# Kernel optimization log

Measured on AMD Instinct MI355X. Metric: run time of the kernel, lower is better.

## Reference

```python
import jax, jax.numpy as jnp
import numpy as np

B, HW, D, CL, K, V, NL, H = 16, 4096, 512, 768, 512, 512, 32, 8
EPS = 1e-5

def conv1d(x, w, b):
    # 1x1 Conv1d: x (B, Cin, L), w (Cout, Cin), b (Cout,)
    return jnp.einsum('oi,bil->bol', w, x) + b[:, None]

def inorm(x):
    # InstanceNorm1d (affine=False, biased var) over the length dim per channel
    m = jnp.mean(x, axis=-1, keepdims=True)
    v = jnp.var(x, axis=-1, keepdims=True)
    return (x - m) / jnp.sqrt(v + EPS)

def _forward(x, l, l_mask, w_vis, b_vis, w_langp, b_langp, w_q, b_q, w_k, b_k,
             w_v, b_v, w_lv, b_lv, w_W, b_W, w_langW, b_langW,
             w_mm, b_mm, w_langmm, b_langmm):
    xt = x.transpose(0, 2, 1)                       # (B, D, HW)
    mask = l_mask.transpose(0, 2, 1)                # (B, 1, NL)
    vis = jax.nn.gelu(conv1d(xt, w_vis, b_vis), approximate=False)      # (B, D, HW)
    lang = jax.nn.gelu(conv1d(l, w_langp, b_langp), approximate=False)  # (B, CL, NL)

    q = inorm(conv1d(xt, w_q, b_q)).transpose(0, 2, 1)   # (B, HW, K)
    k = conv1d(l, w_k, b_k) * mask                       # (B, K, NL)
    v = conv1d(l, w_v, b_v) * mask                       # (B, V, NL)
    lv = inorm(conv1d(xt, w_lv, b_lv))                   # (B, CL, HW)

    q = q.reshape(B, HW, H, K // H).transpose(0, 2, 1, 3)   # (B, H, HW, dk)
    k = k.reshape(B, H, K // H, NL)
    v = v.reshape(B, H, V // H, NL)
    lv = lv.reshape(B, H, CL // H, HW)

    # note: scale uses FULL key_channels (as in the torch code), mask bias added once
    sim = jnp.einsum('bhqd,bhdn->bhqn', q, k) * (K ** -0.5)
    sim = sim + (10000.0 * mask[:, :, None, :] - 10000.0)    # (B, H, HW, NL)

    att = jax.nn.softmax(sim, axis=-1)                         # image -> lang
    latt = jax.nn.softmax(sim.transpose(0, 1, 3, 2), axis=-1)  # lang -> image

    lang_out = jnp.einsum('bhnq,bhcq->bhcn', latt, lv).reshape(B, CL, NL) * mask
    lang_out = inorm(conv1d(lang_out, w_langW, b_langW))       # (B, CL, NL)

    out = jnp.einsum('bhqn,bhdn->bqhd', att, v).reshape(B, HW, V)
    vis_out = inorm(conv1d(out.transpose(0, 2, 1), w_W, b_W))  # (B, V, HW)

    mm = jax.nn.gelu(conv1d(vis * vis_out, w_mm, b_mm), approximate=False)
    lang_mm = jax.nn.gelu(conv1d(lang * lang_out, w_langmm, b_langmm), approximate=False)
    return mm.transpose(0, 2, 1), lang_mm.transpose(0, 2, 1)   # (B,HW,V), (B,NL,CL)

def setup_inputs():
    key = jax.random.key(0)
    ks = jax.random.split(key, 24)
    inp = {}
    inp['x'] = jax.random.normal(ks[0], (B, HW, D), jnp.float32)
    inp['l'] = jax.random.normal(ks[1], (B, CL, NL), jnp.float32)
    lengths = jax.random.randint(ks[2], (B, 1), 5, NL + 1)
    inp['l_mask'] = (jnp.arange(NL)[None, :] < lengths).astype(jnp.float32)[:, :, None]
    specs = [('vis', D, D), ('langp', CL, CL), ('q', K, D), ('k', K, CL),
             ('v', V, CL), ('lv', CL, D), ('W', V, V), ('langW', CL, CL),
             ('mm', V, V), ('langmm', CL, CL)]
    for i, (n, o, ci) in enumerate(specs):
        inp['w_' + n] = jax.random.normal(ks[3 + 2 * i], (o, ci), jnp.float32) / float(np.sqrt(ci))
        inp['b_' + n] = jax.random.normal(ks[4 + 2 * i], (o,), jnp.float32) * 0.01
    return inp

def reference(x, l, l_mask, w_vis, b_vis, w_langp, b_langp, w_q, b_q, w_k, b_k,
              w_v, b_v, w_lv, b_lv, w_W, b_W, w_langW, b_langW,
              w_mm, b_mm, w_langmm, b_langmm):
    return _forward(x, l, l_mask, w_vis, b_vis, w_langp, b_langp, w_q, b_q, w_k, b_k,
                    w_v, b_v, w_lv, b_lv, w_W, b_W, w_langW, b_langW,
                    w_mm, b_mm, w_langmm, b_langmm)
```

## Files before the change

kernel.cpp:

```cpp
#include <hip/hip_runtime.h>
#include <cstdint>
#include <cstddef>


typedef __bf16 bf16x8 __attribute__((ext_vector_type(8)));
typedef float f32x4 __attribute__((ext_vector_type(4)));
typedef unsigned short ushort8 __attribute__((ext_vector_type(8)));
typedef unsigned short us4 __attribute__((ext_vector_type(4)));

__device__ __forceinline__ float bf2f(unsigned short u) {
  union { unsigned int i; float f; } c; c.i = ((unsigned int)u) << 16; return c.f;
}
__device__ __forceinline__ unsigned short f2bf(float f) {
  union { float f; unsigned int i; } c; c.f = f;
  unsigned int r = c.i + 0x7FFFu + ((c.i >> 16) & 1u);
  return (unsigned short)(r >> 16);
}
__device__ __forceinline__ float gelu_f(float x) {
  return 0.5f * x * (1.f + erff(x * 0.70710678118654752f));
}
__device__ __forceinline__ void gload16(const void* g, void* l) {
  __builtin_amdgcn_global_load_lds(
      (__attribute__((address_space(1))) unsigned int*)g,
      (__attribute__((address_space(3))) unsigned int*)l, 16, 0, 0);
}

constexpr size_t OFF_SRQ  = 0;
constexpr size_t OFF_SRLV = OFF_SRQ  + (size_t)16*512*2*4;
constexpr size_t OFF_SRW  = OFF_SRLV + (size_t)16*768*2*4;
constexpr size_t OFF_LACC = OFF_SRW  + (size_t)16*512*2*4;
constexpr size_t SZ_ZERO  = OFF_LACC + (size_t)16*768*32*4;
constexpr size_t OFF_STQ  = SZ_ZERO;
constexpr size_t OFF_STLV = OFF_STQ  + (size_t)16*512*2*4;
constexpr size_t OFF_STW  = OFF_STLV + (size_t)16*768*2*4;
constexpr size_t OFF_KBUF = OFF_STW  + (size_t)16*512*2*4;
constexpr size_t OFF_VBUF = OFF_KBUF + (size_t)16*512*32*4;
constexpr size_t OFF_LANG = OFF_VBUF + (size_t)16*512*32*4;
constexpr size_t OFF_LMX  = OFF_LANG + (size_t)16*768*32*4;
constexpr size_t OFF_LSM  = OFF_LMX  + (size_t)128*32*4;
constexpr size_t OFF_LNORM= OFF_LSM  + (size_t)128*32*4;
constexpr size_t OFF_P2   = OFF_LNORM+ (size_t)16*768*32*4;
constexpr size_t OFF_PMX  = OFF_P2   + (size_t)16*768*32*4;
constexpr size_t OFF_PSM  = OFF_PMX  + (size_t)32*128*32*4;
constexpr size_t OFF_WB   = OFF_PSM  + (size_t)32*128*32*4;
constexpr size_t OFF_Q    = OFF_WB   + (size_t)1441792*2;
constexpr size_t OFF_LV   = OFF_Q    + (size_t)65536*512*2;
constexpr size_t OFF_SIMB = OFF_LV   + (size_t)65536*768*2;

__global__ __launch_bounds__(256) void cvt_bf16(const float* __restrict__ src,
                                                unsigned short* __restrict__ dst, int n8)
{
  int i = blockIdx.x * 256 + threadIdx.x;
  if (i >= n8) return;
  const f32x4* s = (const f32x4*)(src + (size_t)i * 8);
  f32x4 a = s[0], b = s[1];
  ushort8 o;
#pragma unroll
  for (int j = 0; j < 4; ++j) { o[j] = f2bf(a[j]); o[j + 4] = f2bf(b[j]); }
  *(ushort8*)(dst + (size_t)i * 8) = o;
}

template<bool GELU, bool STATS, bool OUTF32>
__global__ __launch_bounds__(256) void gemm_bt(
    const unsigned short* __restrict__ A, const unsigned short* __restrict__ Wb,
    const float* __restrict__ bias, void* __restrict__ Yout,
    float* __restrict__ statsraw, int N, int Kd)
{
  __shared__ __align__(16) unsigned short As[128 * 64];
  __shared__ __align__(16) unsigned short Bs[128 * 64];
  const int t = threadIdx.x;
  const int wave = t >> 6, lane = t & 63;
  const int ln = lane & 15, quad = lane >> 4;
  const int m0 = blockIdx.x * 128, n0 = blockIdx.y * 128;
  const int wm = (wave >> 1) * 64, wn = (wave & 1) * 64;
  const f32x4 fzero = {0.f, 0.f, 0.f, 0.f};
  f32x4 acc[4][4];
#pragma unroll
  for (int i = 0; i < 4; ++i)
#pragma unroll
    for (int j = 0; j < 4; ++j) acc[i][j] = fzero;
  const int lrow = lane >> 3;
  const int lch  = lane & 7;

  for (int k0 = 0; k0 < Kd; k0 += 64) {
#pragma unroll
    for (int it = 0; it < 4; ++it) {
      int g = wave * 4 + it;
      int row = g * 8 + lrow;
      gload16(A  + (size_t)(m0 + row) * Kd + k0 + lch * 8, &As[g * 512]);
      gload16(Wb + (size_t)(n0 + row) * Kd + k0 + lch * 8, &Bs[g * 512]);
    }
    __syncthreads();
#pragma unroll
    for (int kk = 0; kk < 64; kk += 32) {
      int c = (kk >> 3) + quad;
      bf16x8 af[4], bfr[4];
#pragma unroll
      for (int i = 0; i < 4; ++i)
        af[i] = *(const bf16x8*)&As[(wm + i * 16 + ln) * 64 + c * 8];
#pragma unroll
      for (int j = 0; j < 4; ++j)
        bfr[j] = *(const bf16x8*)&Bs[(wn + j * 16 + ln) * 64 + c * 8];
#pragma unroll
      for (int i = 0; i < 4; ++i)
#pragma unroll
        for (int j = 0; j < 4; ++j)
          acc[i][j] = __builtin_amdgcn_mfma_f32_16x16x32_bf16(af[i], bfr[j], acc[i][j], 0, 0, 0);
    }
    __syncthreads();
  }
  float bb[4];
#pragma unroll
  for (int j = 0; j < 4; ++j) bb[j] = bias[n0 + wn + j * 16 + ln];
#pragma unroll
  for (int i = 0; i < 4; ++i)
#pragma unroll
    for (int j = 0; j < 4; ++j)
#pragma unroll
      for (int r = 0; r < 4; ++r) {
        float v = acc[i][j][r] + bb[j];
        if (GELU) v = gelu_f(v);
        acc[i][j][r] = v;
        size_t row = (size_t)(m0 + wm + i * 16 + quad * 4 + r);
        size_t idx = row * N + (n0 + wn + j * 16 + ln);
        if (OUTF32) ((float*)Yout)[idx] = v;
        else ((unsigned short*)Yout)[idx] = f2bf(v);
      }
  if (STATS) {
    float* cs = (float*)As;
    cs[t] = 0.f;
    __syncthreads();
#pragma unroll
    for (int j = 0; j < 4; ++j) {
      float s = 0.f, s2 = 0.f;
#pragma unroll
      for (int i = 0; i < 4; ++i)
#pragma unroll
        for (int r = 0; r < 4; ++r) { float v = acc[i][j][r]; s += v; s2 += v * v; }
      int cl = wn + j * 16 + ln;
      atomicAdd(&cs[cl], s);
      atomicAdd(&cs[128 + cl], s2);
    }
    __syncthreads();
    int bIdx = m0 >> 12;
    if (t < 128) atomicAdd(&statsraw[((size_t)bIdx * N + n0 + t) * 2], cs[t]);
    else atomicAdd(&statsraw[((size_t)bIdx * N + n0 + (t - 128)) * 2 + 1], cs[t]);
  }
}

__global__ void finalize_stats(const float* __restrict__ raw, float* __restrict__ st,
                               int n, float invc) {
  int i = blockIdx.x * 256 + threadIdx.x;
  if (i >= n) return;
  float s = raw[2 * i], s2 = raw[2 * i + 1];
  float m = s * invc;
  float v = fmaxf(s2 * invc - m * m, 0.f);
  st[2 * i] = m;
  st[2 * i + 1] = rsqrtf(v + 1e-5f);
}

template<int EPI>
__global__ __launch_bounds__(256) void sconv(
    const float* __restrict__ l, const float* __restrict__ w,
    const float* __restrict__ bias, const float* __restrict__ lmask,
    float* __restrict__ out, int O, int Cin)
{
  int b = blockIdx.x, og = blockIdx.y;
  int ol = threadIdx.x >> 5, n = threadIdx.x & 31;
  int o = og * 8 + ol;
  const float* lb = l + (size_t)b * Cin * 32 + n;
  const float* wr = w + (size_t)o * Cin;
  float s = 0.f;
#pragma unroll 4
  for (int i = 0; i < Cin; ++i) s += wr[i] * lb[(size_t)i * 32];
  s += bias[o];
  if (EPI == 0) s *= lmask[b * 32 + n];
  else s = gelu_f(s);
  out[((size_t)b * O + o) * 32 + n] = s;
}

__global__ __launch_bounds__(256) void simattv_kernel(
    const unsigned short* __restrict__ qraw, const float* __restrict__ stq,
    const float* __restrict__ kbuf, const float* __restrict__ vbuf,
    const float* __restrict__ lmask,
    unsigned short* __restrict__ simb, unsigned short* __restrict__ outb,
    float* __restrict__ pmx, float* __restrict__ psm)
{
  __shared__ __align__(16) unsigned short kThi[32][72];
  __shared__ __align__(16) unsigned short kTlo[32][72];
  __shared__ __align__(16) unsigned short vshi[64][40];
  __shared__ __align__(16) unsigned short vslo[64][40];
  __shared__ __align__(16) unsigned short pq[4][32][40];
  __shared__ float sm[64], srs[64], cb[32];
  __shared__ float wmax[4][32], wsum[4][32];

  const int qc = blockIdx.x, q0 = qc * 128, h = blockIdx.y, b = blockIdx.z;
  const int bh = b * 8 + h;
  const int t = threadIdx.x;
  const int wv = t >> 6, lane = t & 63, ln = lane & 15, quad = lane >> 4;
  const float scale = 0.04419417382415922f;

  if (t < 64) {
    sm[t]  = stq[(b * 512 + h * 64 + t) * 2];
    srs[t] = stq[(b * 512 + h * 64 + t) * 2 + 1] * scale;
  }
  __syncthreads();

  const float* kb = kbuf + ((size_t)b * 512 + h * 64) * 32;
  const float* vb = vbuf + ((size_t)b * 512 + h * 64) * 32;
  for (int e = t; e < 2048; e += 256) {
    int d = e >> 5, n = e & 31;
    float kv = kb[e] * srs[d];
    unsigned short khi = f2bf(kv);
    kThi[n][d] = khi;
    kTlo[n][d] = f2bf(kv - bf2f(khi));
    float vv = vb[e];
    unsigned short vhi = f2bf(vv);
    vshi[d][n] = vhi;
    vslo[d][n] = f2bf(vv - bf2f(vhi));
  }
  if (t < 32) {
    float s = 0.f;
#pragma unroll 8
    for (int d = 0; d < 64; ++d) s += sm[d] * srs[d] * kb[d * 32 + t];
    cb[t] = 10000.f * (lmask[b * 32 + t] - 1.f) - s;
  }

  const unsigned short* qbase = qraw + ((size_t)(b * 4096) + q0 + wv * 32) * 512 + h * 64;
  bf16x8 qfr[2][2];
#pragma unroll
  for (int qf = 0; qf < 2; ++qf)
#pragma unroll
    for (int kf = 0; kf < 2; ++kf)
      qfr[qf][kf] = *(const bf16x8*)(qbase + (size_t)(qf * 16 + ln) * 512 + kf * 32 + quad * 8);
  __syncthreads();

  const f32x4 fz = {0.f, 0.f, 0.f, 0.f};
  f32x4 accS[2][2] = {{fz, fz}, {fz, fz}};
#pragma unroll
  for (int kf = 0; kf < 2; ++kf) {
#pragma unroll
    for (int nf = 0; nf < 2; ++nf) {
      bf16x8 kh = *(const bf16x8*)&kThi[nf * 16 + ln][kf * 32 + quad * 8];
      bf16x8 kl = *(const bf16x8*)&kTlo[nf * 16 + ln][kf * 32 + quad * 8];
#pragma unroll
      for (int qf = 0; qf < 2; ++qf) {
        accS[qf][nf] = __builtin_amdgcn_mfma_f32_16x16x32_bf16(qfr[qf][kf], kh, accS[qf][nf], 0, 0, 0);
        accS[qf][nf] = __builtin_amdgcn_mfma_f32_16x16x32_bf16(qfr[qf][kf], kl, accS[qf][nf], 0, 0, 0);
      }
    }
  }
  float cb0 = cb[ln], cb1 = cb[16 + ln];
#pragma unroll
  for (int qf = 0; qf < 2; ++qf)
#pragma unroll
    for (int r = 0; r < 4; ++r) {
      accS[qf][0][r] += cb0;
      accS[qf][1][r] += cb1;
    }
  {
    unsigned short* sgb = simb + ((size_t)bh * 4096 + q0 + wv * 32) * 32;
#pragma unroll
    for (int qf = 0; qf < 2; ++qf)
#pragma unroll
      for (int r = 0; r < 4; ++r) {
        size_t rowo = (size_t)(qf * 16 + quad * 4 + r) * 32;
        sgb[rowo + ln]      = f2bf(accS[qf][0][r]);
        sgb[rowo + 16 + ln] = f2bf(accS[qf][1][r]);
      }
  }
#pragma unroll
  for (int nf = 0; nf < 2; ++nf) {
    float m = accS[0][nf][0];
#pragma unroll
    for (int r = 1; r < 4; ++r) m = fmaxf(m, accS[0][nf][r]);
#pragma unroll
    for (int r = 0; r < 4; ++r) m = fmaxf(m, accS[1][nf][r]);
    m = fmaxf(m, __shfl_xor(m, 16));
    m = fmaxf(m, __shfl_xor(m, 32));
    float s = 0.f;
#pragma unroll
    for (int qf = 0; qf < 2; ++qf)
#pragma unroll
      for (int r = 0; r < 4; ++r) s += __expf(accS[qf][nf][r] - m);
    s += __shfl_xor(s, 16);
    s += __shfl_xor(s, 32);
    if (quad == 0) { wmax[wv][nf * 16 + ln] = m; wsum[wv][nf * 16 + ln] = s; }
  }
#pragma unroll
  for (int qf = 0; qf < 2; ++qf) {
#pragma unroll
    for (int r = 0; r < 4; ++r) {
      float a0 = accS[qf][0][r], a1 = accS[qf][1][r];
      float m = fmaxf(a0, a1);
      m = fmaxf(m, __shfl_xor(m, 1));
      m = fmaxf(m, __shfl_xor(m, 2));
      m = fmaxf(m, __shfl_xor(m, 4));
      m = fmaxf(m, __shfl_xor(m, 8));
      float e0 = __expf(a0 - m), e1 = __expf(a1 - m);
      float s = e0 + e1;
      s += __shfl_xor(s, 1);
      s += __shfl_xor(s, 2);
      s += __shfl_xor(s, 4);
      s += __shfl_xor(s, 8);
      float inv = 1.f / s;
      int row = qf * 16 + quad * 4 + r;
      pq[wv][row][ln]      = f2bf(e0 * inv);
      pq[wv][row][16 + ln] = f2bf(e1 * inv);
    }
  }
  __syncthreads();
  bf16x8 vfh[4], vfl[4];
#pragma unroll
  for (int mf = 0; mf < 4; ++mf) {
    vfh[mf] = *(const bf16x8*)&vshi[mf * 16 + ln][quad * 8];
    vfl[mf] = *(const bf16x8*)&vslo[mf * 16 + ln][quad * 8];
  }
#pragma unroll
  for (int nf = 0; nf < 2; ++nf) {
    bf16x8 pb = *(const bf16x8*)&pq[wv][nf * 16 + ln][quad * 8];
    f32x4 accO[4] = {fz, fz, fz, fz};
#pragma unroll
    for (int mf = 0; mf < 4; ++mf) {
      accO[mf] = __builtin_amdgcn_mfma_f32_16x16x32_bf16(vfh[mf], pb, accO[mf], 0, 0, 0);
      accO[mf] = __builtin_amdgcn_mfma_f32_16x16x32_bf16(vfl[mf], pb, accO[mf], 0, 0, 0);
    }
    unsigned short* op = outb + ((size_t)(b * 4096) + q0 + wv * 32 + nf * 16 + ln) * 512 + h * 64;
#pragma unroll
    for (int mf = 0; mf < 4; ++mf) {
      us4 o;
#pragma unroll
      for (int r = 0; r < 4; ++r) o[r] = f2bf(accO[mf][r]);
      *(us4*)(op + mf * 16 + quad * 4) = o;
    }
  }
  __syncthreads();
  if (t < 32) {
    float M = wmax[0][t], S = wsum[0][t];
#pragma unroll
    for (int g = 1; g < 4; ++g) {
      float m2 = wmax[g][t], s2 = wsum[g][t];
      if (m2 > M) { S = S * __expf(M - m2) + s2; M = m2; }
      else S += s2 * __expf(m2 - M);
    }
    pmx[((size_t)qc * 128 + bh) * 32 + t] = M;
    psm[((size_t)qc * 128 + bh) * 32 + t] = S;
  }
}

__global__ __launch_bounds__(256) void latt_merge(const float* __restrict__ pmx,
                                                  const float* __restrict__ psm,
                                                  float* __restrict__ lmx,
                                                  float* __restrict__ lsm)
{
  int i = blockIdx.x * 256 + threadIdx.x;
  int bh = i >> 5, n = i & 31;
  float M = -1e30f, S = 0.f;
#pragma unroll 4
  for (int c = 0; c < 32; ++c) {
    float m2 = pmx[((size_t)c * 128 + bh) * 32 + n];
    float s2 = psm[((size_t)c * 128 + bh) * 32 + n];
    if (m2 > M) { S = S * __expf(M - m2) + s2; M = m2; }
    else S += s2 * __expf(m2 - M);
  }
  lmx[bh * 32 + n] = M;
  lsm[bh * 32 + n] = S;
}

__global__ __launch_bounds__(256) void langout_acc_kernel(
    const unsigned short* __restrict__ simb, const float* __restrict__ lmx,
    const float* __restrict__ lsm, const unsigned short* __restrict__ lvraw,
    const float* __restrict__ stlv, float* __restrict__ lacc)
{
  __shared__ __align__(16) float pt[64][32];
  __shared__ __align__(16) float lvt[64][96];
  __shared__ float cm[96], cr[96], lm[32], li[32];
  int bh = blockIdx.x, b = bh >> 3, h = bh & 7;
  int qs0 = blockIdx.y * 512;
  int t = threadIdx.x;
  if (t < 96) { cm[t] = stlv[(b * 768 + h * 96 + t) * 2]; cr[t] = stlv[(b * 768 + h * 96 + t) * 2 + 1]; }
  else if (t >= 128 && t < 160) {
    int n = t - 128;
    lm[n] = lmx[bh * 32 + n];
    li[n] = 1.f / lsm[bh * 32 + n];
  }
  __syncthreads();
  int n = t & 31, cg = t >> 5;
  float acc[12];
#pragma unroll
  for (int r = 0; r < 12; ++r) acc[r] = 0.f;
  for (int c0 = 0; c0 < 512; c0 += 64) {
    if (c0) __syncthreads();
#pragma unroll
    for (int i = 0; i < 8; ++i) {
      int e = t + 256 * i;
      int ql = e >> 5, nn = e & 31;
      float x = bf2f(simb[((size_t)bh * 4096 + qs0 + c0 + ql) * 32 + nn]);
      pt[ql][nn] = __expf(x - lm[nn]) * li[nn];
    }
#pragma unroll
    for (int i = 0; i < 24; ++i) {
      int e = t + 256 * i;
      int ql = e / 96, cc = e % 96;
      float v = bf2f(lvraw[((size_t)(b * 4096) + qs0 + c0 + ql) * 768 + h * 96 + cc]);
      lvt[ql][cc] = (v - cm[cc]) * cr[cc];
    }
    __syncthreads();
    for (int q = 0; q < 64; ++q) {
      float pv = pt[q][n];
      const f32x4* lp = (const f32x4*)&lvt[q][cg * 12];
      f32x4 a0 = lp[0], a1 = lp[1], a2 = lp[2];
      acc[0] += pv * a0[0]; acc[1] += pv * a0[1]; acc[2]  += pv * a0[2]; acc[3]  += pv * a0[3];
      acc[4] += pv * a1[0]; acc[5] += pv * a1[1]; acc[6]  += pv * a1[2]; acc[7]  += pv * a1[3];
      acc[8] += pv * a2[0]; acc[9] += pv * a2[1]; acc[10] += pv * a2[2]; acc[11] += pv * a2[3];
    }
  }
#pragma unroll
  for (int r = 0; r < 12; ++r)
    atomicAdd(&lacc[((size_t)b * 768 + h * 96 + cg * 12 + r) * 32 + n], acc[r]);
}

__global__ __launch_bounds__(256) void prod_kernel(
    const unsigned short* __restrict__ visb, const unsigned short* __restrict__ wraw,
    const float* __restrict__ stw, unsigned short* __restrict__ P)
{
  size_t idx = ((size_t)blockIdx.x * 256 + threadIdx.x) * 8;
  int b = (int)(idx >> 21);
  int c = (int)(idx & 511);
  ushort8 vv = *(const ushort8*)&visb[idx];
  ushort8 wv = *(const ushort8*)&wraw[idx];
  ushort8 pv;
#pragma unroll
  for (int i = 0; i < 8; ++i) {
    float mean = stw[(b * 512 + c + i) * 2], rs = stw[(b * 512 + c + i) * 2 + 1];
    pv[i] = f2bf(bf2f(vv[i]) * ((bf2f(wv[i]) - mean) * rs));
  }
  *(ushort8*)&P[idx] = pv;
}

__global__ __launch_bounds__(256) void langW_kernel(
    const float* __restrict__ lacc, const float* __restrict__ w,
    const float* __restrict__ bias, const float* __restrict__ lmask,
    float* __restrict__ lnorm)
{
  int b = blockIdx.x, og = blockIdx.y;
  int ol = threadIdx.x >> 5, n = threadIdx.x & 31;
  int o = og * 8 + ol;
  const float* ab = lacc + (size_t)b * 768 * 32 + n;
  const float* wr = w + (size_t)o * 768;
  float s = 0.f;
#pragma unroll 4
  for (int i = 0; i < 768; ++i) s += wr[i] * ab[(size_t)i * 32];
  float y = s * lmask[b * 32 + n] + bias[o];
  float m = y;
#pragma unroll
  for (int off = 16; off >= 1; off >>= 1) m += __shfl_xor(m, off);
  m *= (1.f / 32.f);
  float d = y - m;
  float vv = d * d;
#pragma unroll
  for (int off = 16; off >= 1; off >>= 1) vv += __shfl_xor(vv, off);
  vv *= (1.f / 32.f);
  lnorm[((size_t)b * 768 + o) * 32 + n] = d * rsqrtf(vv + 1e-5f);
}

__global__ __launch_bounds__(256) void p2_kernel(const float* __restrict__ a,
                                                 const float* __restrict__ b,
                                                 float* __restrict__ o, int n) {
  int i = blockIdx.x * 256 + threadIdx.x;
  if (i < n) o[i] = a[i] * b[i];
}

__global__ __launch_bounds__(256) void langmm_kernel(
    const float* __restrict__ p2, const float* __restrict__ w,
    const float* __restrict__ bias, float* __restrict__ out1)
{
  int b = blockIdx.x, og = blockIdx.y;
  int ol = threadIdx.x >> 5, n = threadIdx.x & 31;
  int o = og * 8 + ol;
  const float* pb = p2 + (size_t)b * 768 * 32 + n;
  const float* wr = w + (size_t)o * 768;
  float s = 0.f;
#pragma unroll 4
  for (int i = 0; i < 768; ++i) s += wr[i] * pb[(size_t)i * 32];
  s = gelu_f(s + bias[o]);
  __shared__ float tile[8][32];
  tile[ol][n] = s;
  __syncthreads();
  int nn = threadIdx.x >> 3, cl = threadIdx.x & 7;
  out1[((size_t)b * 32 + nn) * 768 + og * 8 + cl] = tile[cl][nn];
}

extern "C" void kernel_launch(void* const* d_in, const int* in_sizes, int n_in,
                              void* d_out, int out_size, void* d_ws, size_t ws_size,
                              hipStream_t stream)
{
  (void)in_sizes; (void)n_in; (void)out_size; (void)ws_size;
  const float* x       = (const float*)d_in[0];
  const float* l       = (const float*)d_in[1];
  const float* lmask   = (const float*)d_in[2];
  const float* w_vis   = (const float*)d_in[3];
  const float* b_vis   = (const float*)d_in[4];
  const float* w_langp = (const float*)d_in[5];
  const float* b_langp = (const float*)d_in[6];
  const float* w_q     = (const float*)d_in[7];
  const float* b_q     = (const float*)d_in[8];
  const float* w_k     = (const float*)d_in[9];
  const float* b_k     = (const float*)d_in[10];
  const float* w_v     = (const float*)d_in[11];
  const float* b_v     = (const float*)d_in[12];
  const float* w_lv    = (const float*)d_in[13];
  const float* b_lv    = (const float*)d_in[14];
  const float* w_W     = (const float*)d_in[15];
  const float* b_W     = (const float*)d_in[16];
  const float* w_langW = (const float*)d_in[17];
  const float* b_langW = (const float*)d_in[18];
  const float* w_mm    = (const float*)d_in[19];
  const float* b_mm    = (const float*)d_in[20];
  const float* w_langmm= (const float*)d_in[21];
  const float* b_langmm= (const float*)d_in[22];

  char* ws = (char*)d_ws;
  float* srq  = (float*)(ws + OFF_SRQ);
  float* srlv = (float*)(ws + OFF_SRLV);
  float* srw  = (float*)(ws + OFF_SRW);
  float* lacc = (float*)(ws + OFF_LACC);
  float* stq  = (float*)(ws + OFF_STQ);
  float* stlv = (float*)(ws + OFF_STLV);
  float* stw  = (float*)(ws + OFF_STW);
  float* kbuf = (float*)(ws + OFF_KBUF);
  float* vbuf = (float*)(ws + OFF_VBUF);
  float* lang = (float*)(ws + OFF_LANG);
  float* lmx  = (float*)(ws + OFF_LMX);
  float* lsm  = (float*)(ws + OFF_LSM);
  float* lnorm= (float*)(ws + OFF_LNORM);
  float* p2   = (float*)(ws + OFF_P2);
  float* pmx  = (float*)(ws + OFF_PMX);
  float* psm  = (float*)(ws + OFF_PSM);
  unsigned short* wb    = (unsigned short*)(ws + OFF_WB);
  unsigned short* wbvis = wb;
  unsigned short* wbq   = wb + 262144;
  unsigned short* wblv  = wb + 524288;
  unsigned short* wbW   = wb + 917504;
  unsigned short* wbmm  = wb + 1179648;
  unsigned short* qraw  = (unsigned short*)(ws + OFF_Q);
  unsigned short* lvraw = (unsigned short*)(ws + OFF_LV);
  unsigned short* wraw  = (unsigned short*)(ws + OFF_LV);
  unsigned short* simb  = (unsigned short*)(ws + OFF_SIMB);
  float* out0 = (float*)d_out;
  float* out1 = out0 + (size_t)16 * 4096 * 512;
  unsigned short* visb = (unsigned short*)d_out;
  unsigned short* xb   = (unsigned short*)d_out + 33554432;

  hipMemsetAsync(ws, 0, SZ_ZERO, stream);

  cvt_bf16<<<16384, 256, 0, stream>>>(x, xb, 4194304);
  cvt_bf16<<<128, 256, 0, stream>>>(w_vis, wbvis, 32768);
  cvt_bf16<<<128, 256, 0, stream>>>(w_q,   wbq,   32768);
  cvt_bf16<<<192, 256, 0, stream>>>(w_lv,  wblv,  49152);
  cvt_bf16<<<128, 256, 0, stream>>>(w_W,   wbW,   32768);
  cvt_bf16<<<128, 256, 0, stream>>>(w_mm,  wbmm,  32768);

  sconv<1><<<dim3(16, 96), 256, 0, stream>>>(l, w_langp, b_langp, lmask, lang, 768, 768);
  sconv<0><<<dim3(16, 64), 256, 0, stream>>>(l, w_k, b_k, lmask, kbuf, 512, 768);
  sconv<0><<<dim3(16, 64), 256, 0, stream>>>(l, w_v, b_v, lmask, vbuf, 512, 768);

  gemm_bt<true,  false, false><<<dim3(512, 4), 256, 0, stream>>>(xb, wbvis, b_vis, visb, nullptr, 512, 512);
  gemm_bt<false, true,  false><<<dim3(512, 4), 256, 0, stream>>>(xb, wbq,   b_q,   qraw,  srq,   512, 512);
  gemm_bt<false, true,  false><<<dim3(512, 6), 256, 0, stream>>>(xb, wblv,  b_lv,  lvraw, srlv,  768, 512);
  finalize_stats<<<32, 256, 0, stream>>>(srq,  stq,  16 * 512, 1.f / 4096.f);
  finalize_stats<<<48, 256, 0, stream>>>(srlv, stlv, 16 * 768, 1.f / 4096.f);

  simattv_kernel<<<dim3(32, 8, 16), 256, 0, stream>>>(qraw, stq, kbuf, vbuf, lmask, simb, qraw, pmx, psm);
  latt_merge<<<16, 256, 0, stream>>>(pmx, psm, lmx, lsm);
  langout_acc_kernel<<<dim3(128, 8), 256, 0, stream>>>(simb, lmx, lsm, lvraw, stlv, lacc);

  gemm_bt<false, true,  false><<<dim3(512, 4), 256, 0, stream>>>(qraw, wbW, b_W, wraw, srw, 512, 512);
  finalize_stats<<<32, 256, 0, stream>>>(srw, stw, 16 * 512, 1.f / 4096.f);
  prod_kernel<<<16384, 256, 0, stream>>>(visb, wraw, stw, qraw);
  gemm_bt<true,  false, true ><<<dim3(512, 4), 256, 0, stream>>>(qraw, wbmm, b_mm, out0, nullptr, 512, 512);

  langW_kernel<<<dim3(16, 96), 256, 0, stream>>>(lacc, w_langW, b_langW, lmask, lnorm);
  p2_kernel<<<1536, 256, 0, stream>>>(lang, lnorm, p2, 16 * 768 * 32);
  langmm_kernel<<<dim3(16, 96), 256, 0, stream>>>(p2, w_langmm, b_langmm, out1);
}
```

Measured before the change: 1.305 ms.

## Fuse vis/q/lv projection GEMMs into one launch and add XCD-aware block swizzle

The three 1x1-conv GEMMs that all read the bf16 input x are merged into a single kernel over a concatenated weight matrix with 14 column tiles. Each tile picks its bias, epilogue (GELU or instance-norm stats) and output buffer by segment. This removes two launches and lets the shared A tiles be reused across output columns, instead of streaming x three times. All GEMMs also switch to a 1-D grid with an XCD-aware swizzle so neighbouring tiles land on the same chiplet for better L2 reuse. The cost is a per-tile branchy epilogue, plus reliance on the converted weights being laid out contiguously.

```diff
diff --git a/kernel.cpp b/kernel.cpp
--- a/kernel.cpp
+++ b/kernel.cpp
@@ -23,6 +23,11 @@
   __builtin_amdgcn_global_load_lds(
       (__attribute__((address_space(1))) unsigned int*)g,
       (__attribute__((address_space(3))) unsigned int*)l, 16, 0, 0);
+}
+__device__ __forceinline__ int xcd_swizzle(int orig, int nwg) {
+  int qd = nwg >> 3, r = nwg & 7;
+  int xcd = orig & 7, idx = orig >> 3;
+  return (xcd < r ? xcd * (qd + 1) : r * (qd + 1) + (xcd - r) * qd) + idx;
 }
 
 constexpr size_t OFF_SRQ  = 0;
@@ -64,14 +69,16 @@
 __global__ __launch_bounds__(256) void gemm_bt(
     const unsigned short* __restrict__ A, const unsigned short* __restrict__ Wb,
     const float* __restrict__ bias, void* __restrict__ Yout,
-    float* __restrict__ statsraw, int N, int Kd)
+    float* __restrict__ statsraw, int N, int Kd, int nbn)
 {
   __shared__ __align__(16) unsigned short As[128 * 64];
   __shared__ __align__(16) unsigned short Bs[128 * 64];
   const int t = threadIdx.x;
   const int wave = t >> 6, lane = t & 63;
   const int ln = lane & 15, quad = lane >> 4;
-  const int m0 = blockIdx.x * 128, n0 = blockIdx.y * 128;
+  const int wgid = xcd_swizzle(blockIdx.x, gridDim.x);
+  const int mt = wgid / nbn, nt = wgid - mt * nbn;
+  const int m0 = mt * 128, n0 = nt * 128;
   const int wm = (wave >> 1) * 64, wn = (wave & 1) * 64;
   const f32x4 fzero = {0.f, 0.f, 0.f, 0.f};
   f32x4 acc[4][4];
@@ -145,6 +152,102 @@
     int bIdx = m0 >> 12;
     if (t < 128) atomicAdd(&statsraw[((size_t)bIdx * N + n0 + t) * 2], cs[t]);
     else atomicAdd(&statsraw[((size_t)bIdx * N + n0 + (t - 128)) * 2 + 1], cs[t]);
+  }
+}
+
+__global__ __launch_bounds__(256) void gemm_fused3(
+    const unsigned short* __restrict__ A, const unsigned short* __restrict__ Wcat,
+    const float* __restrict__ b_vis, const float* __restrict__ b_q, const float* __restrict__ b_lv,
+    unsigned short* __restrict__ visb, unsigned short* __restrict__ qout,
+    unsigned short* __restrict__ lvout, float* __restrict__ srq, float* __restrict__ srlv)
+{
+  constexpr int NBN = 14, Kd = 512;
+  __shared__ __align__(16) unsigned short As[128 * 64];
+  __shared__ __align__(16) unsigned short Bs[128 * 64];
+  const int t = threadIdx.x;
+  const int wave = t >> 6, lane = t & 63;
+  const int ln = lane & 15, quad = lane >> 4;
+  const int wgid = xcd_swizzle(blockIdx.x, gridDim.x);
+  const int mt = wgid / NBN, nt = wgid - mt * NBN;
+  const int m0 = mt * 128, n0 = nt * 128;
+  const int wm = (wave >> 1) * 64, wn = (wave & 1) * 64;
+  const f32x4 fzero = {0.f, 0.f, 0.f, 0.f};
+  f32x4 acc[4][4];
+#pragma unroll
+  for (int i = 0; i < 4; ++i)
+#pragma unroll
+    for (int j = 0; j < 4; ++j) acc[i][j] = fzero;
+  const int lrow = lane >> 3;
+  const int lch  = lane & 7;
+
+  for (int k0 = 0; k0 < Kd; k0 += 64) {
+#pragma unroll
+    for (int it = 0; it < 4; ++it) {
+      int g = wave * 4 + it;
+      int row = g * 8 + lrow;
+      gload16(A    + (size_t)(m0 + row) * Kd + k0 + lch * 8, &As[g * 512]);
+      gload16(Wcat + (size_t)(n0 + row) * Kd + k0 + lch * 8, &Bs[g * 512]);
+    }
+    __syncthreads();
+#pragma unroll
+    for (int kk = 0; kk < 64; kk += 32) {
+      int c = (kk >> 3) + quad;
+      bf16x8 af[4], bfr[4];
+#pragma unroll
+      for (int i = 0; i < 4; ++i)
+        af[i] = *(const bf16x8*)&As[(wm + i * 16 + ln) * 64 + c * 8];
+#pragma unroll
+      for (int j = 0; j < 4; ++j)
+        bfr[j] = *(const bf16x8*)&Bs[(wn + j * 16 + ln) * 64 + c * 8];
+#pragma unroll
+      for (int i = 0; i < 4; ++i)
+#pragma unroll
+        for (int j = 0; j < 4; ++j)
+          acc[i][j] = __builtin_amdgcn_mfma_f32_16x16x32_bf16(af[i], bfr[j], acc[i][j], 0, 0, 0);
+    }
+    __syncthreads();
+  }
+  int seg = (nt < 4) ? 0 : (nt < 8 ? 1 : 2);
+  const float* bias = (seg == 0) ? b_vis : (seg == 1 ? b_q : b_lv);
+  unsigned short* Y = (seg == 0) ? visb : (seg == 1 ? qout : lvout);
+  float* statsraw   = (seg == 1) ? srq : srlv;
+  const int nbase   = n0 - ((seg == 0) ? 0 : (seg == 1 ? 512 : 1024));
+  const int Nseg    = (seg == 2) ? 768 : 512;
+
+  float bb[4];
+#pragma unroll
+  for (int j = 0; j < 4; ++j) bb[j] = bias[nbase + wn + j * 16 + ln];
+#pragma unroll
+  for (int i = 0; i < 4; ++i)
+#pragma unroll
+    for (int j = 0; j < 4; ++j)
+#pragma unroll
+      for (int r = 0; r < 4; ++r) {
+        float v = acc[i][j][r] + bb[j];
+        if (seg == 0) v = gelu_f(v);
+        acc[i][j][r] = v;
+        size_t row = (size_t)(m0 + wm + i * 16 + quad * 4 + r);
+        Y[row * Nseg + (nbase + wn + j * 16 + ln)] = f2bf(v);
+      }
+  if (seg != 0) {
+    float* cs = (float*)As;
+    cs[t] = 0.f;
+    __syncthreads();
+#pragma unroll
+    for (int j = 0; j < 4; ++j) {
+      float s = 0.f, s2 = 0.f;
+#pragma unroll
+      for (int i = 0; i < 4; ++i)
+#pragma unroll
+        for (int r = 0; r < 4; ++r) { float v = acc[i][j][r]; s += v; s2 += v * v; }
+      int cl = wn + j * 16 + ln;
+      atomicAdd(&cs[cl], s);
+      atomicAdd(&cs[128 + cl], s2);
+    }
+    __syncthreads();
+    int bIdx = m0 >> 12;
+    if (t < 128) atomicAdd(&statsraw[((size_t)bIdx * Nseg + nbase + t) * 2], cs[t]);
+    else atomicAdd(&statsraw[((size_t)bIdx * Nseg + nbase + (t - 128)) * 2 + 1], cs[t]);
   }
 }
 
@@ -565,9 +668,8 @@
   sconv<0><<<dim3(16, 64), 256, 0, stream>>>(l, w_k, b_k, lmask, kbuf, 512, 768);
   sconv<0><<<dim3(16, 64), 256, 0, stream>>>(l, w_v, b_v, lmask, vbuf, 512, 768);
 
-  gemm_bt<true,  false, false><<<dim3(512, 4), 256, 0, stream>>>(xb, wbvis, b_vis, visb, nullptr, 512, 512);
-  gemm_bt<false, true,  false><<<dim3(512, 4), 256, 0, stream>>>(xb, wbq,   b_q,   qraw,  srq,   512, 512);
-  gemm_bt<false, true,  false><<<dim3(512, 6), 256, 0, stream>>>(xb, wblv,  b_lv,  lvraw, srlv,  768, 512);
+  gemm_fused3<<<512 * 14, 256, 0, stream>>>(xb, wb, b_vis, b_q, b_lv,
+                                            visb, qraw, lvraw, srq, srlv);
   finalize_stats<<<32, 256, 0, stream>>>(srq,  stq,  16 * 512, 1.f / 4096.f);
   finalize_stats<<<48, 256, 0, stream>>>(srlv, stlv, 16 * 768, 1.f / 4096.f);
 
@@ -575,10 +677,10 @@
   latt_merge<<<16, 256, 0, stream>>>(pmx, psm, lmx, lsm);
   langout_acc_kernel<<<dim3(128, 8), 256, 0, stream>>>(simb, lmx, lsm, lvraw, stlv, lacc);
 
-  gemm_bt<false, true,  false><<<dim3(512, 4), 256, 0, stream>>>(qraw, wbW, b_W, wraw, srw, 512, 512);
+  gemm_bt<false, true,  false><<<512 * 4, 256, 0, stream>>>(qraw, wbW, b_W, wraw, srw, 512, 512, 4);
   finalize_stats<<<32, 256, 0, stream>>>(srw, stw, 16 * 512, 1.f / 4096.f);
   prod_kernel<<<16384, 256, 0, stream>>>(visb, wraw, stw, qraw);
-  gemm_bt<true,  false, true ><<<dim3(512, 4), 256, 0, stream>>>(qraw, wbmm, b_mm, out0, nullptr, 512, 512);
+  gemm_bt<true,  false, true ><<<512 * 4, 256, 0, stream>>>(qraw, wbmm, b_mm, out0, nullptr, 512, 512, 4);
 
   langW_kernel<<<dim3(16, 96), 256, 0, stream>>>(lacc, w_langW, b_langW, lmask, lnorm);
   p2_kernel<<<1536, 256, 0, stream>>>(lang, lnorm, p2, 16 * 768 * 32);
```

Result: faster. 1.279 ms (-2.0%).
